# Kernel tuning notes

Measured on AMD Instinct MI355X. Metric: run time of the kernel, lower is better.

## Reference

```python
import jax, jax.numpy as jnp
import numpy as np


def _compute_deltas(ts, m):
    """Affine time-decay recurrence: delta_0 = 0; for t>=1:
    delta_t = gap_t + (1 - m_{t-1}) * delta_{t-1}, with gap broadcast over features.
    ts: [b, s] timestamps, m: [b, s, f] float 0/1 mask. Returns [b, s, f]."""
    b, s, f = m.shape
    gaps = ts[:, 1:] - ts[:, :-1]          # [b, s-1]
    a = 1.0 - m[:, :-1, :]                 # [b, s-1, f] decay coefficient

    def step(d, inp):
        g_t, a_t = inp                      # g_t: [b], a_t: [b, f]
        d = g_t[:, None] + a_t * d
        return d, d

    gT = jnp.swapaxes(gaps, 0, 1)          # [s-1, b]
    aT = jnp.swapaxes(a, 0, 1)             # [s-1, b, f]
    _, ds = jax.lax.scan(step, jnp.zeros((b, f), ts.dtype), (gT, aT))
    ds = jnp.swapaxes(ds, 0, 1)            # [b, s-1, f]
    return jnp.concatenate([jnp.zeros((b, 1, f), ts.dtype), ds], axis=1)


def setup_inputs() -> dict:
    key = jax.random.key(0)
    k1, k2, k3 = jax.random.split(key, 3)
    b, s, f = 32, 2048, 768
    # monotonically increasing timestamps (cumsum of positive gaps)
    gaps = jax.random.uniform(k1, (b, s), minval=1.0, maxval=60.0, dtype=jnp.float32)
    timestamps = jnp.cumsum(gaps, axis=1)
    encoded_data = jax.random.normal(k2, (b, s, f), dtype=jnp.float32)
    masks = jax.random.randint(k3, (b, s, f), 0, 2, dtype=jnp.int32)
    return {"timestamps": timestamps, "encoded_data": encoded_data, "masks": masks}


def reference(timestamps, encoded_data, masks):
    """JAX translation of _prepare_brits_data. Returns stacked
    [forward_deltas, backward_deltas, backward_X] of shape [3, b, s, f].
    (forward X / masks are pass-through inputs; backward mask is flip(masks).)"""
    m = masks.astype(timestamps.dtype)
    forward_deltas = _compute_deltas(timestamps, m)
    ts_b = jnp.flip(timestamps, axis=1)
    m_b = jnp.flip(m, axis=1)
    backward_deltas = jnp.abs(_compute_deltas(ts_b, m_b))
    x_b = jnp.flip(encoded_data, axis=1)
    return jnp.stack([forward_deltas, backward_deltas, x_b], axis=0)
```

## Files before the change

### kernel.cpp

```cpp
#include <hip/hip_runtime.h>
#include <stdint.h>

static constexpr int B = 32, S = 2048, F = 768;
static constexpr int SC = 64;
static constexpr int NSC = S / SC;
static constexpr int F4 = F / 4;
static constexpr int FT = F4;

__global__ __launch_bounds__(FT) void fusedK(const float* __restrict__ ts,
                                             const float4* __restrict__ x,
                                             const int4* __restrict__ masks,
                                             float* __restrict__ out) {
    const int blk = blockIdx.x;
    const int pair = blk >> 1;
    const int b  = pair >> 5;
    const int sc = pair & (NSC - 1);
    const int g0 = sc * SC;
    const int j  = threadIdx.x;
    const size_t N4 = (size_t)B * S * F4;

    if (blk & 1) {
        const float4* xb = x + (size_t)b * S * F4 + j;
        float4* o2 = reinterpret_cast<float4*>(out) + 2 * N4 + (size_t)(b * S + g0) * F4 + j;
        #pragma unroll 8
        for (int k = 0; k < SC; ++k) {
            o2[(size_t)k * F4] = xb[(size_t)(S - 1 - g0 - k) * F4];
        }
        return;
    }

    const float* tsb = ts + (size_t)b * S;
    const int4* mbase = masks + (size_t)b * S * F4 + j;

    __shared__ float tss[SC];
    if (j < SC) tss[j] = tsb[g0 + j];
    __syncthreads();

    uint32_t a0 = 0, a1 = 0, a2 = 0, a3 = 0;
    uint32_t c0 = 0, c1 = 0, c2 = 0, c3 = 0;
    #pragma unroll
    for (int g = 0; g < 8; ++g) {
        int4 mv[8];
        #pragma unroll
        for (int q = 0; q < 8; ++q) mv[q] = mbase[(size_t)(g0 + g * 8 + q) * F4];
        #pragma unroll
        for (int q = 0; q < 8; ++q) {
            const int k = g * 8 + q;
            const uint32_t bit = 1u << (k & 31);
            if (k < 32) {
                if (mv[q].x) a0 |= bit;
                if (mv[q].y) a1 |= bit;
                if (mv[q].z) a2 |= bit;
                if (mv[q].w) a3 |= bit;
            } else {
                if (mv[q].x) c0 |= bit;
                if (mv[q].y) c1 |= bit;
                if (mv[q].z) c2 |= bit;
                if (mv[q].w) c3 |= bit;
            }
        }
    }

    float t0v = tsb[0];
    float p0 = t0v, p1 = t0v, p2 = t0v, p3 = t0v;
    if (g0 > 0) {
        unsigned um = 0xFu;
        int r = g0 - 1;
        while (um && r >= 0) {
            int rl = (r - 7 > 0) ? r - 7 : 0;
            int nn = r - rl + 1;
            int4 mv[8];
            #pragma unroll
            for (int q = 0; q < 8; ++q) if (q < nn) mv[q] = mbase[(size_t)(r - q) * F4];
            #pragma unroll
            for (int q = 0; q < 8; ++q) if (q < nn) {
                float t = tsb[r - q];
                if ((um & 1u) && mv[q].x) { p0 = t; um &= ~1u; }
                if ((um & 2u) && mv[q].y) { p1 = t; um &= ~2u; }
                if ((um & 4u) && mv[q].z) { p2 = t; um &= ~4u; }
                if ((um & 8u) && mv[q].w) { p3 = t; um &= ~8u; }
            }
            r = rl - 1;
        }
    }

    float tev = tsb[S - 1];
    float n0 = tev, n1 = tev, n2 = tev, n3 = tev;
    if (g0 + SC < S) {
        unsigned um = 0xFu;
        int r = g0 + SC;
        while (um && r < S) {
            int rh = (r + 7 < S - 1) ? r + 7 : S - 1;
            int nn = rh - r + 1;
            int4 mv[8];
            #pragma unroll
            for (int q = 0; q < 8; ++q) if (q < nn) mv[q] = mbase[(size_t)(r + q) * F4];
            #pragma unroll
            for (int q = 0; q < 8; ++q) if (q < nn) {
                float t = tsb[r + q];
                if ((um & 1u) && mv[q].x) { n0 = t; um &= ~1u; }
                if ((um & 2u) && mv[q].y) { n1 = t; um &= ~2u; }
                if ((um & 4u) && mv[q].z) { n2 = t; um &= ~4u; }
                if ((um & 8u) && mv[q].w) { n3 = t; um &= ~8u; }
            }
            r = rh + 1;
        }
    }

    float4* o0 = reinterpret_cast<float4*>(out) + (size_t)(b * S + g0) * F4 + j;
    #pragma unroll
    for (int k = 0; k < 32; ++k) {
        float t = tss[k];
        o0[(size_t)k * F4] = make_float4(t - p0, t - p1, t - p2, t - p3);
        const uint32_t bit = 1u << k;
        if (a0 & bit) p0 = t;
        if (a1 & bit) p1 = t;
        if (a2 & bit) p2 = t;
        if (a3 & bit) p3 = t;
    }
    #pragma unroll
    for (int k = 32; k < 64; ++k) {
        float t = tss[k];
        o0[(size_t)k * F4] = make_float4(t - p0, t - p1, t - p2, t - p3);
        const uint32_t bit = 1u << (k - 32);
        if (c0 & bit) p0 = t;
        if (c1 & bit) p1 = t;
        if (c2 & bit) p2 = t;
        if (c3 & bit) p3 = t;
    }

    float4* o1b = reinterpret_cast<float4*>(out) + N4 + (size_t)b * S * F4 + j;
    #pragma unroll
    for (int k = 63; k >= 32; --k) {
        float t = tss[k];
        size_t fr = (size_t)(S - 1 - g0 - k) * F4;
        o1b[fr] = make_float4(n0 - t, n1 - t, n2 - t, n3 - t);
        const uint32_t bit = 1u << (k - 32);
        if (c0 & bit) n0 = t;
        if (c1 & bit) n1 = t;
        if (c2 & bit) n2 = t;
        if (c3 & bit) n3 = t;
    }
    #pragma unroll
    for (int k = 31; k >= 0; --k) {
        float t = tss[k];
        size_t fr = (size_t)(S - 1 - g0 - k) * F4;
        o1b[fr] = make_float4(n0 - t, n1 - t, n2 - t, n3 - t);
        const uint32_t bit = 1u << k;
        if (a0 & bit) n0 = t;
        if (a1 & bit) n1 = t;
        if (a2 & bit) n2 = t;
        if (a3 & bit) n3 = t;
    }
}

extern "C" void kernel_launch(void* const* d_in, const int* in_sizes, int n_in,
                              void* d_out, int out_size, void* d_ws, size_t ws_size,
                              hipStream_t stream) {
    const float* ts    = (const float*)d_in[0];
    const float4* x    = (const float4*)d_in[1];
    const int4*  masks = (const int4*)d_in[2];
    float* out = (float*)d_out;
    fusedK<<<2 * B * NSC, FT, 0, stream>>>(ts, x, masks, out);
}
```

Measured before the change: 238.0 us.

## Split flip-copy into separate grid-stride kernel and use nontemporal stores

Moves the reversed-X copy out of the fused kernel's odd blocks into its own grid-stride kernel, so the delta kernel launches only delta blocks. All output stores, and the copy's loads, now use nontemporal builtins to avoid polluting cache with streaming data. This adds a second kernel launch, serialises the copy after the delta work on the same stream, and adds per-element index division in the copy loop.

```diff
diff --git a/kernel.cpp b/kernel.cpp
--- a/kernel.cpp
+++ b/kernel.cpp
@@ -7,27 +7,21 @@
 static constexpr int F4 = F / 4;
 static constexpr int FT = F4;
 
-__global__ __launch_bounds__(FT) void fusedK(const float* __restrict__ ts,
-                                             const float4* __restrict__ x,
+typedef float v4f __attribute__((ext_vector_type(4)));
+
+__device__ __forceinline__ v4f mk4(float a, float b, float c, float d) {
+    v4f v; v.x = a; v.y = b; v.z = c; v.w = d; return v;
+}
+
+__global__ __launch_bounds__(FT) void deltaK(const float* __restrict__ ts,
                                              const int4* __restrict__ masks,
                                              float* __restrict__ out) {
-    const int blk = blockIdx.x;
-    const int pair = blk >> 1;
+    const int pair = blockIdx.x;
     const int b  = pair >> 5;
     const int sc = pair & (NSC - 1);
     const int g0 = sc * SC;
     const int j  = threadIdx.x;
     const size_t N4 = (size_t)B * S * F4;
-
-    if (blk & 1) {
-        const float4* xb = x + (size_t)b * S * F4 + j;
-        float4* o2 = reinterpret_cast<float4*>(out) + 2 * N4 + (size_t)(b * S + g0) * F4 + j;
-        #pragma unroll 8
-        for (int k = 0; k < SC; ++k) {
-            o2[(size_t)k * F4] = xb[(size_t)(S - 1 - g0 - k) * F4];
-        }
-        return;
-    }
 
     const float* tsb = ts + (size_t)b * S;
     const int4* mbase = masks + (size_t)b * S * F4 + j;
@@ -107,11 +101,11 @@
         }
     }
 
-    float4* o0 = reinterpret_cast<float4*>(out) + (size_t)(b * S + g0) * F4 + j;
+    v4f* o0 = reinterpret_cast<v4f*>(out) + (size_t)(b * S + g0) * F4 + j;
     #pragma unroll
     for (int k = 0; k < 32; ++k) {
         float t = tss[k];
-        o0[(size_t)k * F4] = make_float4(t - p0, t - p1, t - p2, t - p3);
+        __builtin_nontemporal_store(mk4(t - p0, t - p1, t - p2, t - p3), &o0[(size_t)k * F4]);
         const uint32_t bit = 1u << k;
         if (a0 & bit) p0 = t;
         if (a1 & bit) p1 = t;
@@ -121,7 +115,7 @@
     #pragma unroll
     for (int k = 32; k < 64; ++k) {
         float t = tss[k];
-        o0[(size_t)k * F4] = make_float4(t - p0, t - p1, t - p2, t - p3);
+        __builtin_nontemporal_store(mk4(t - p0, t - p1, t - p2, t - p3), &o0[(size_t)k * F4]);
         const uint32_t bit = 1u << (k - 32);
         if (c0 & bit) p0 = t;
         if (c1 & bit) p1 = t;
@@ -129,12 +123,12 @@
         if (c3 & bit) p3 = t;
     }
 
-    float4* o1b = reinterpret_cast<float4*>(out) + N4 + (size_t)b * S * F4 + j;
+    v4f* o1b = reinterpret_cast<v4f*>(out) + N4 + (size_t)b * S * F4 + j;
     #pragma unroll
     for (int k = 63; k >= 32; --k) {
         float t = tss[k];
         size_t fr = (size_t)(S - 1 - g0 - k) * F4;
-        o1b[fr] = make_float4(n0 - t, n1 - t, n2 - t, n3 - t);
+        __builtin_nontemporal_store(mk4(n0 - t, n1 - t, n2 - t, n3 - t), &o1b[fr]);
         const uint32_t bit = 1u << (k - 32);
         if (c0 & bit) n0 = t;
         if (c1 & bit) n1 = t;
@@ -145,7 +139,7 @@
     for (int k = 31; k >= 0; --k) {
         float t = tss[k];
         size_t fr = (size_t)(S - 1 - g0 - k) * F4;
-        o1b[fr] = make_float4(n0 - t, n1 - t, n2 - t, n3 - t);
+        __builtin_nontemporal_store(mk4(n0 - t, n1 - t, n2 - t, n3 - t), &o1b[fr]);
         const uint32_t bit = 1u << k;
         if (a0 & bit) n0 = t;
         if (a1 & bit) n1 = t;
@@ -154,12 +148,28 @@
     }
 }
 
+static constexpr int CPY_BLOCKS = 2048;
+__global__ __launch_bounds__(256) void copyK(const v4f* __restrict__ x,
+                                             v4f* __restrict__ o2) {
+    const size_t N4 = (size_t)B * S * F4;
+    const size_t stride = (size_t)CPY_BLOCKS * 256;
+    for (size_t i = (size_t)blockIdx.x * 256 + threadIdx.x; i < N4; i += stride) {
+        size_t row = i / F4;
+        size_t f   = i - row * F4;
+        size_t t   = row & (S - 1);
+        size_t src = (row - t + (S - 1 - t)) * F4 + f;
+        __builtin_nontemporal_store(__builtin_nontemporal_load(&x[src]), &o2[i]);
+    }
+}
+
 extern "C" void kernel_launch(void* const* d_in, const int* in_sizes, int n_in,
                               void* d_out, int out_size, void* d_ws, size_t ws_size,
                               hipStream_t stream) {
     const float* ts    = (const float*)d_in[0];
-    const float4* x    = (const float4*)d_in[1];
+    const v4f* x       = (const v4f*)d_in[1];
     const int4*  masks = (const int4*)d_in[2];
     float* out = (float*)d_out;
-    fusedK<<<2 * B * NSC, FT, 0, stream>>>(ts, x, masks, out);
+    const size_t N4 = (size_t)B * S * F4;
+    deltaK<<<B * NSC, FT, 0, stream>>>(ts, masks, out);
+    copyK<<<CPY_BLOCKS, 256, 0, stream>>>(x, reinterpret_cast<v4f*>(out) + 2 * N4);
 }
```

Result: faster. 194.1 us (-18.5%).
